# Performance work log

Measured on AMD Instinct MI355X. Metric: run time of the kernel, lower is better.

The kernel has to match this reference:

```python
import jax, jax.numpy as jnp
import numpy as np

B, T, E = 2, 2048, 1024
H = 16
D = E // H  # head_dim = 64


def setup_inputs() -> dict:
    key = jax.random.key(0)
    ks = jax.random.split(key, 9)
    s = 1.0 / np.sqrt(E)
    inp = {"x": jax.random.normal(ks[0], (B, T, E), dtype=jnp.float32)}
    # Linear params (torch nn.Linear: y = x @ W.T + b)
    inp["Wq"] = jax.random.uniform(ks[1], (E, E), jnp.float32, -s, s)
    inp["bq"] = jax.random.uniform(ks[2], (E,), jnp.float32, -s, s)
    inp["Wk"] = jax.random.uniform(ks[3], (E, E), jnp.float32, -s, s)
    inp["bk"] = jax.random.uniform(ks[4], (E,), jnp.float32, -s, s)
    inp["Wv"] = jax.random.uniform(ks[5], (E, E), jnp.float32, -s, s)
    inp["bv"] = jax.random.uniform(ks[6], (E,), jnp.float32, -s, s)
    inp["Wo"] = jax.random.uniform(ks[7], (E, E), jnp.float32, -s, s)
    inp["bo"] = jax.random.uniform(ks[8], (E,), jnp.float32, -s, s)
    return inp


def reference(x, Wq, bq, Wk, bk, Wv, bv, Wo, bo):
    # QKV projections, reshape to [B, H, T, D]
    def split_heads(y):
        return y.reshape(B, T, H, D).transpose(0, 2, 1, 3)

    Q = split_heads(x @ Wq.T + bq)
    K = split_heads(x @ Wk.T + bk)
    V = split_heads(x @ Wv.T + bv)

    scale = 1.0 / jnp.sqrt(jnp.asarray(D, x.dtype))
    scores = jnp.einsum("bhqd,bhkd->bhqk", Q, K) * scale  # [B,H,T,T]
    attn = jax.nn.softmax(scores, axis=-1)
    out = jnp.einsum("bhqk,bhkd->bhqd", attn, V)  # [B,H,T,D]
    out = out.transpose(0, 2, 1, 3).reshape(B, T, E)
    # dropout is identity in eval mode
    return out @ Wo.T + bo
```

## Files before the change

### kernel.cpp

```cpp
#include <hip/hip_runtime.h>
#include <math.h>

#define BB 2
#define TT 2048
#define EE 1024
#define HH 16
#define DD 64
#define MM (BB*TT)
#define KK EE

typedef short bf16x8 __attribute__((ext_vector_type(8)));
typedef float f32x4  __attribute__((ext_vector_type(4)));
typedef float f32x16 __attribute__((ext_vector_type(16)));
typedef unsigned int u32x4 __attribute__((ext_vector_type(4)));

__device__ __forceinline__ unsigned short f2bf(float f) {
  unsigned int u = __float_as_uint(f);
  u = (u + 0x7FFFu + ((u >> 16) & 1u)) >> 16;
  return (unsigned short)u;
}

__device__ __forceinline__ unsigned int cvtpk(float lo, float hi) {
  unsigned int r;
  asm("v_cvt_pk_bf16_f32 %0, %1, %2" : "=v"(r) : "v"(lo), "v"(hi));
  return r;
}

__device__ __forceinline__ void plswap(unsigned int &a, unsigned int &b) {
  asm("v_permlane32_swap_b32 %0, %1" : "+v"(a), "+v"(b));
}

__device__ __forceinline__ void async16(const void* g, void* l) {
  __builtin_amdgcn_global_load_lds(
      (const __attribute__((address_space(1))) unsigned int*)g,
      (__attribute__((address_space(3))) unsigned int*)l, 16, 0, 0);
}

__global__ __launch_bounds__(256) void to_bf16(
    const float* __restrict__ x,  const float* __restrict__ wq,
    const float* __restrict__ wk, const float* __restrict__ wv,
    const float* __restrict__ wo,
    unsigned short* __restrict__ xh, unsigned short* __restrict__ wcat,
    unsigned short* __restrict__ woh)
{
  int c = blockIdx.x * 256 + threadIdx.x;
  const float* src; unsigned short* dst; int off;
  if (c < 1048576) { src = x; dst = xh; off = c; }
  else {
    int r = c - 1048576;
    int w = r >> 18;
    off = r & 262143;
    if      (w == 0) { src = wq; dst = wcat; }
    else if (w == 1) { src = wk; dst = wcat + (1 << 20); }
    else if (w == 2) { src = wv; dst = wcat + (2 << 20); }
    else             { src = wo; dst = woh; }
  }
  float4 v = ((const float4*)src)[off];
  ushort4 h;
  h.x = f2bf(v.x); h.y = f2bf(v.y); h.z = f2bf(v.z); h.w = f2bf(v.w);
  ((ushort4*)dst)[off] = h;
}

template<int MODE>
__global__ __launch_bounds__(512, 6) void gemm_bf16(
    const unsigned short* __restrict__ A, const unsigned short* __restrict__ B,
    const float* __restrict__ b0p, const float* __restrict__ b1p,
    const float* __restrict__ b2p,
    unsigned short* __restrict__ oq, unsigned short* __restrict__ ok,
    unsigned short* __restrict__ ov, float* __restrict__ ofp, float qscale)
{
  constexpr int NT = (MODE == 0) ? 128 : 64;
  constexpr int JN = NT / 32;
  constexpr int BROWS = NT * 32;
  constexpr int TOT = (MODE == 0) ? 16 : 12;
  __shared__ unsigned short S[12288 + 3 * BROWS];

  const int tid  = threadIdx.x;
  const int lane = tid & 63;
  const int wv   = tid >> 6;
  const int col  = lane & 15;
  const int quad = lane >> 4;
  const int wm = (wv & 3) * 32;
  const int wn = (wv >> 2) * (NT / 2);
  const int m0 = blockIdx.x * 128;
  const int n0 = blockIdx.y * NT;

  const int srow = lane >> 2;
  const int sw16 = (((lane & 3) ^ ((lane >> 2) & 3) ^ (lane >> 4)) << 3);
  const int fswA = ((quad ^ (col & 3) ^ (col >> 2)) << 3);

  auto stage = [&](int kt, int slot) {
#pragma unroll
    for (int s = 0; s < 2; ++s) {
      const int t = wv * 2 + s;
      if (t < TOT) {
        const unsigned short* src; int rb, g0, loff;
        if (t < 8) { src = A; rb = t * 16;       g0 = m0; loff = slot * 4096; }
        else       { src = B; rb = (t - 8) * 16; g0 = n0; loff = 12288 + slot * BROWS; }
        async16(src + (size_t)(g0 + rb + srow) * KK + kt + sw16,
                S + loff + rb * 32);
      }
    }
  };

  f32x4 acc[2][JN];
  const f32x4 z = {0.f, 0.f, 0.f, 0.f};
#pragma unroll
  for (int i = 0; i < 2; ++i)
#pragma unroll
    for (int j = 0; j < JN; ++j) acc[i][j] = z;

  stage(0, 0);

#define GBODY(T, SL, S2, DOSTAGE, VMC) do {                                   \
    if (DOSTAGE) stage(((T) + 1) * 32, S2);                                   \
    asm volatile("s_waitcnt vmcnt(" #VMC ")" ::: "memory");                   \
    __builtin_amdgcn_sched_barrier(0);                                        \
    __builtin_amdgcn_s_barrier();                                             \
    __builtin_amdgcn_sched_barrier(0);                                        \
    const unsigned short* Asb = S + (SL) * 4096;                              \
    const unsigned short* Bsb = S + 12288 + (SL) * BROWS;                     \
    bf16x8 bfr[JN];                                                           \
    _Pragma("unroll")                                                         \
    for (int j = 0; j < JN; ++j)                                              \
      bfr[j] = *(const bf16x8*)(Bsb + (wn + j * 16 + col) * 32 + fswA);       \
    _Pragma("unroll")                                                         \
    for (int i = 0; i < 2; ++i) {                                             \
      bf16x8 af = *(const bf16x8*)(Asb + (wm + i * 16 + col) * 32 + fswA);    \
      _Pragma("unroll")                                                       \
      for (int j = 0; j < JN; ++j)                                            \
        acc[i][j] = __builtin_amdgcn_mfma_f32_16x16x32_bf16(af, bfr[j], acc[i][j], 0, 0, 0); \
    }                                                                         \
  } while (0)

  for (int t = 0; t < 30; t += 3) {
    GBODY(t + 0, 0, 1, 1, 2);
    GBODY(t + 1, 1, 2, 1, 2);
    GBODY(t + 2, 2, 0, 1, 2);
  }
  GBODY(30, 0, 1, 1, 2);
  GBODY(31, 1, 0, 0, 0);
#undef GBODY

  unsigned short* Cs = S;
  if (MODE == 0) {
    __syncthreads();
    const int region = n0 >> 10;
    const float* bias = (region == 0) ? b0p : (region == 1) ? b1p : b2p;
    const float scl = (region == 0) ? qscale : 1.0f;
    const int nlbase = n0 & 1023;
    const int h0 = nlbase >> 6;
    const int b = m0 >> 11, t0 = m0 & (TT - 1);
    if (region < 2) {
#pragma unroll
      for (int i = 0; i < 2; ++i)
#pragma unroll
        for (int j = 0; j < 4; ++j) {
          const int nt = wn + j * 16 + col;
          const float bs = bias[nlbase + nt];
#pragma unroll
          for (int r = 0; r < 4; ++r) {
            const int mt = wm + i * 16 + quad * 4 + r;
            Cs[mt * 136 + nt] = f2bf((acc[i][j][r] + bs) * scl);
          }
        }
      __syncthreads();
      unsigned short* dst = (region == 0) ? oq : ok;
#pragma unroll
      for (int s = 0; s < 4; ++s) {
        const int u = s * 512 + tid;
        const int mt = u >> 4, hs = (u >> 3) & 1, ch = u & 7;
        const size_t g = ((size_t)(b * HH + h0 + hs) * TT + t0 + mt) * DD + ch * 8;
        *(uint4*)(dst + g) = *(const uint4*)(Cs + mt * 136 + hs * 64 + ch * 8);
      }
    } else {
#pragma unroll
      for (int i = 0; i < 2; ++i)
#pragma unroll
        for (int j = 0; j < 4; ++j) {
          const int nt = wn + j * 16 + col;
          const float bs = bias[nlbase + nt];
          ushort4 pk;
          pk.x = f2bf(acc[i][j][0] + bs);
          pk.y = f2bf(acc[i][j][1] + bs);
          pk.z = f2bf(acc[i][j][2] + bs);
          pk.w = f2bf(acc[i][j][3] + bs);
          *(ushort4*)(Cs + nt * 136 + wm + i * 16 + quad * 4) = pk;
        }
      __syncthreads();
#pragma unroll
      for (int s = 0; s < 4; ++s) {
        const int u = s * 512 + tid;
        const int nt = u >> 4, ch = u & 15;
        const int d = nt & 63, hs = nt >> 6;
        const size_t g = ((size_t)(b * HH + h0 + hs) * DD + d) * TT + t0 + ch * 8;
        *(uint4*)(ov + g) = *(const uint4*)(Cs + nt * 136 + ch * 8);
      }
    }
  } else {
#pragma unroll
    for (int i = 0; i < 2; ++i) {
#pragma unroll
      for (int j = 0; j < JN; ++j) {
        const int n = n0 + wn + j * 16 + col;
        const float bs = b0p[n];
#pragma unroll
        for (int r = 0; r < 4; ++r) {
          const int m = m0 + wm + i * 16 + quad * 4 + r;
          ofp[(size_t)m * EE + n] = acc[i][j][r] + bs;
        }
      }
    }
  }
}

__global__ __launch_bounds__(512, 6) void gemm_out(
    const unsigned short* __restrict__ A, const unsigned short* __restrict__ B,
    const float* __restrict__ bias, float* __restrict__ ofp)
{
  __shared__ unsigned short S[24576];

  const int tid  = threadIdx.x;
  const int lane = tid & 63;
  const int wv   = tid >> 6;
  const int col  = lane & 15;
  const int quad = lane >> 4;
  const int wm = (wv & 3) * 32;
  const int wn = (wv >> 2) * 32;
  const int m0 = blockIdx.x * 128;
  const int n0 = blockIdx.y * 64;

  const int srow = lane >> 2;
  const int sw16 = (((lane & 3) ^ ((lane >> 2) & 3) ^ (lane >> 4)) << 3);
  const int fswA = ((quad ^ (col & 3) ^ (col >> 2)) << 3);

  auto stage = [&](int kt, int slot) {
#pragma unroll
    for (int s = 0; s < 2; ++s) {
      const int t = wv * 2 + s;
      if (t < 12) {
        const unsigned short* src; int rb, g0, loff;
        if (t < 8) { src = A; rb = t * 16;       g0 = m0; loff = slot * 4096; }
        else       { src = B; rb = (t - 8) * 16; g0 = n0; loff = 16384 + slot * 2048; }
        async16(src + (size_t)(g0 + rb + srow) * KK + kt + sw16,
                S + loff + rb * 32);
      }
    }
  };

  f32x4 acc[2][2];
  const f32x4 z = {0.f, 0.f, 0.f, 0.f};
#pragma unroll
  for (int i = 0; i < 2; ++i)
#pragma unroll
    for (int j = 0; j < 2; ++j) acc[i][j] = z;

  stage(0, 0);
  stage(32, 1);

#define GCOMP(SL) do {                                                        \
    const unsigned short* Asb = S + (SL) * 4096;                              \
    const unsigned short* Bsb = S + 16384 + (SL) * 2048;                      \
    bf16x8 b0 = *(const bf16x8*)(Bsb + (wn + col) * 32 + fswA);               \
    bf16x8 b1 = *(const bf16x8*)(Bsb + (wn + 16 + col) * 32 + fswA);          \
    _Pragma("unroll")                                                         \
    for (int i = 0; i < 2; ++i) {                                             \
      bf16x8 af = *(const bf16x8*)(Asb + (wm + i * 16 + col) * 32 + fswA);    \
      acc[i][0] = __builtin_amdgcn_mfma_f32_16x16x32_bf16(af, b0, acc[i][0], 0, 0, 0); \
      acc[i][1] = __builtin_amdgcn_mfma_f32_16x16x32_bf16(af, b1, acc[i][1], 0, 0, 0); \
    }                                                                         \
} while (0)

#define REGION2(T, SLa, SLb, SSa, SSb, DOSTAGE, VMC) do {                     \
    asm volatile("s_waitcnt vmcnt(" #VMC ")" ::: "memory");                   \
    __builtin_amdgcn_sched_barrier(0);                                        \
    __builtin_amdgcn_s_barrier();                                             \
    __builtin_amdgcn_sched_barrier(0);                                        \
    if (DOSTAGE) { stage(((T) + 2) * 32, SSa); stage(((T) + 3) * 32, SSb); }  \
    GCOMP(SLa);                                                               \
    GCOMP(SLb);                                                               \
} while (0)

  for (int t = 0; t < 28; t += 4) {
    REGION2(t + 0, 0, 1, 2, 3, 1, 0);
    REGION2(t + 2, 2, 3, 0, 1, 1, 0);
  }
  REGION2(28, 0, 1, 2, 3, 1, 0);
  REGION2(30, 2, 3, 0, 1, 0, 0);
#undef REGION2
#undef GCOMP

#pragma unroll
  for (int i = 0; i < 2; ++i) {
#pragma unroll
    for (int j = 0; j < 2; ++j) {
      const int n = n0 + wn + j * 16 + col;
      const float bs = bias[n];
#pragma unroll
      for (int r = 0; r < 4; ++r) {
        const int m = m0 + wm + i * 16 + quad * 4 + r;
        ofp[(size_t)m * EE + n] = acc[i][j][r] + bs;
      }
    }
  }
}

__global__ __launch_bounds__(512, 4) void flash_mfma(
    const unsigned short* __restrict__ Qb, const unsigned short* __restrict__ Kb,
    const unsigned short* __restrict__ Vtb, unsigned short* __restrict__ ctx)
{
  __shared__ unsigned short Qs[128 * 64];
  __shared__ unsigned short Ks[4][64 * 64];
  __shared__ unsigned short Vts[4][64 * 64];

  const int tid  = threadIdx.x;
  const int lane = tid & 63;
  const int wv   = tid >> 6;
  const int lq   = lane & 31;
  const int hf   = lane >> 5;
  const int wq   = wv & 3;
  const int wk2  = wv >> 2;
  const int gid  = blockIdx.x;
  const int bh   = gid & 31;
  const int q0   = (gid >> 5) * 128;

  const unsigned short* Qg = Qb  + (size_t)bh * TT * DD;
  const unsigned short* Kg = Kb  + (size_t)bh * TT * DD;
  const unsigned short* Vg = Vtb + (size_t)bh * DD * TT;

  const int srow = lane >> 3;
  const int swb  = ((lane & 7) ^ (lane >> 3)) << 3;

  const int rbK = wq * 16;
  const bool isK = (wv < 4);
  const int sw0 = swb ^ ((((rbK    ) >> 3) & 7) << 3);
  const int sw1 = swb ^ ((((rbK + 8) >> 3) & 7) << 3);
  const unsigned short* g0 =
      (isK ? Kg + (size_t)(rbK + srow) * DD : Vg + (size_t)(rbK + srow) * TT) + sw0;
  const unsigned short* g1 =
      (isK ? Kg + (size_t)(rbK + 8 + srow) * DD : Vg + (size_t)(rbK + 8 + srow) * TT) + sw1;
  unsigned short* l0 = (isK ? &Ks[0][0] : &Vts[0][0]) + rbK * 64;
  unsigned short* l1 = l0 + 8 * 64;
  const int gstep = isK ? 64 * DD : 64;

  auto stage_kv = [&](int ti, int slot) {
    const size_t go = (size_t)ti * gstep;
    async16(g0 + go, l0 + slot * 4096);
    async16(g1 + go, l1 + slot * 4096);
  };

  const int l7 = lane & 7;
  const int d3 = lq >> 3;
  int koff[4], voff[2][2];
#pragma unroll
  for (int s = 0; s < 4; ++s)
    koff[s] = ((wk2 * 32 + lq) * 64 +
               (((2 * s + hf) ^ l7 ^ ((wk2 * 4 + d3) & 7)) << 3)) * 2;
#pragma unroll
  for (int m = 0; m < 2; ++m)
#pragma unroll
    for (int sg = 0; sg < 2; ++sg)
      voff[m][sg] = ((m * 32 + lq) * 64 +
                     (((wk2 * 4 + 2 * sg + hf) ^ l7 ^ ((m * 4 + d3) & 7)) << 3)) * 2;

#pragma unroll
  for (int s = 0; s < 2; ++s) {
    const int rb = wv * 16 + s * 8;
    const int sq = swb ^ (((rb >> 3) & 7) << 3);
    async16(Qg + (size_t)(q0 + rb + srow) * DD + sq, &Qs[rb * 64]);
  }
  stage_kv(0, 0);
  stage_kv(1, 1);
  __syncthreads();

  bf16x8 aq[4];
#pragma unroll
  for (int s = 0; s < 4; ++s)
    aq[s] = *(const bf16x8*)(Qs + (wq * 32 + lq) * 64 +
                             (((2 * s + hf) ^ l7 ^ ((wq * 4 + d3) & 7)) << 3));

  const f32x16 z16 = {0.f,0.f,0.f,0.f,0.f,0.f,0.f,0.f,
                      0.f,0.f,0.f,0.f,0.f,0.f,0.f,0.f};
  f32x16 o_acc[2];
  o_acc[0] = z16; o_acc[1] = z16;
  float lpart = 0.f;

#define SMPACK(SIN, PA0, PA1) do {                                            \
    {                                                                         \
      float e0 = __builtin_amdgcn_exp2f(SIN[0]);                              \
      float e1 = __builtin_amdgcn_exp2f(SIN[1]);                              \
      float e2 = __builtin_amdgcn_exp2f(SIN[2]);                              \
      float e3 = __builtin_amdgcn_exp2f(SIN[3]);                              \
      float e4 = __builtin_amdgcn_exp2f(SIN[4]);                              \
      float e5 = __builtin_amdgcn_exp2f(SIN[5]);                              \
      float e6 = __builtin_amdgcn_exp2f(SIN[6]);                              \
      float e7 = __builtin_amdgcn_exp2f(SIN[7]);                              \
      lpart += ((e0 + e1) + (e2 + e3)) + ((e4 + e5) + (e6 + e7));             \
      unsigned int a0 = cvtpk(e0, e1), b0 = cvtpk(e4, e5);                    \
      unsigned int a1 = cvtpk(e2, e3), b1 = cvtpk(e6, e7);                    \
      plswap(a0, b0); plswap(a1, b1);                                         \
      u32x4 w = {a0, a1, b0, b1};                                             \
      PA0 = __builtin_bit_cast(bf16x8, w);                                    \
    }                                                                         \
    {                                                                         \
      float e0 = __builtin_amdgcn_exp2f(SIN[8]);                              \
      float e1 = __builtin_amdgcn_exp2f(SIN[9]);                              \
      float e2 = __builtin_amdgcn_exp2f(SIN[10]);                             \
      float e3 = __builtin_amdgcn_exp2f(SIN[11]);                             \
      float e4 = __builtin_amdgcn_exp2f(SIN[12]);                             \
      float e5 = __builtin_amdgcn_exp2f(SIN[13]);                             \
      float e6 = __builtin_amdgcn_exp2f(SIN[14]);                             \
      float e7 = __builtin_amdgcn_exp2f(SIN[15]);                             \
      lpart += ((e0 + e1) + (e2 + e3)) + ((e4 + e5) + (e6 + e7));             \
      unsigned int a0 = cvtpk(e0, e1), b0 = cvtpk(e4, e5);                    \
      unsigned int a1 = cvtpk(e2, e3), b1 = cvtpk(e6, e7);                    \
      plswap(a0, b0); plswap(a1, b1);                                         \
      u32x4 w = {a0, a1, b0, b1};                                             \
      PA1 = __builtin_bit_cast(bf16x8, w);                                    \
    }                                                                         \
} while (0)

#define QKT(SL, SOUT) do {                                                    \
    const char* Kp = (const char*)&Ks[SL][0];                                 \
    bf16x8 ak = *(const bf16x8*)(Kp + koff[0]);                               \
    SOUT = __builtin_amdgcn_mfma_f32_32x32x16_bf16(ak, aq[0], z16, 0, 0, 0);  \
    _Pragma("unroll")                                                         \
    for (int s = 1; s < 4; ++s) {                                             \
      ak = *(const bf16x8*)(Kp + koff[s]);                                    \
      SOUT = __builtin_amdgcn_mfma_f32_32x32x16_bf16(ak, aq[s], SOUT, 0, 0, 0); \
    }                                                                         \
} while (0)

#define PVT(SL, P0, P1) do {                                                  \
    const char* Vp = (const char*)&Vts[SL][0];                                \
    _Pragma("unroll")                                                         \
    for (int m = 0; m < 2; ++m) {                                             \
      bf16x8 v0 = *(const bf16x8*)(Vp + voff[m][0]);                          \
      bf16x8 v1 = *(const bf16x8*)(Vp + voff[m][1]);                          \
      o_acc[m] = __builtin_amdgcn_mfma_f32_32x32x16_bf16(P0, v0, o_acc[m], 0, 0, 0); \
      o_acc[m] = __builtin_amdgcn_mfma_f32_32x32x16_bf16(P1, v1, o_acc[m], 0, 0, 0); \
    }                                                                         \
} while (0)

#define REGION(T, SLa, SLb, SSa, SSb, DOSTAGE) do {                           \
    asm volatile("s_waitcnt vmcnt(0)" ::: "memory");                          \
    __builtin_amdgcn_sched_barrier(0);                                        \
    __builtin_amdgcn_s_barrier();                                             \
    __builtin_amdgcn_sched_barrier(0);                                        \
    if (DOSTAGE) { stage_kv((T) + 2, SSa); stage_kv((T) + 3, SSb); }          \
    f32x16 sa, sb;                                                            \
    __builtin_amdgcn_s_setprio(1);                                            \
    QKT(SLa, sa);                                                             \
    QKT(SLb, sb);                                                             \
    __builtin_amdgcn_s_setprio(0);                                            \
    bf16x8 pa0, pa1, pb0, pb1;                                                \
    SMPACK(sa, pa0, pa1);                                                     \
    __builtin_amdgcn_s_setprio(1);                                            \
    PVT(SLa, pa0, pa1);                                                       \
    __builtin_amdgcn_s_setprio(0);                                            \
    SMPACK(sb, pb0, pb1);                                                     \
    __builtin_amdgcn_s_setprio(1);                                            \
    PVT(SLb, pb0, pb1);                                                       \
    __builtin_amdgcn_s_setprio(0);                                            \
} while (0)

  for (int t = 0; t < 28; t += 4) {
    REGION(t + 0, 0, 1, 2, 3, 1);
    REGION(t + 2, 2, 3, 0, 1, 1);
  }
  REGION(28, 0, 1, 2, 3, 1);
  REGION(30, 2, 3, 0, 1, 0);
#undef REGION
#undef PVT
#undef QKT
#undef SMPACK

  float* Qf = (float*)&Qs[0];
  float* Of = (float*)&Ks[0][0];
  unsigned short* Cs = &Vts[0][0];
  const int bq = bh >> 4, head = bh & 15;

  float lw = lpart + __shfl_xor(lpart, 32);
  if (lane < 32) Qf[wv * 32 + lane] = lw;
  __syncthreads();

  if (wv >= 4) {
#pragma unroll
    for (int m = 0; m < 2; ++m)
#pragma unroll
      for (int r = 0; r < 16; ++r) {
        const int ql = (r & 3) + 8 * (r >> 2) + 4 * hf;
        Of[wq * 2048 + ql * 64 + m * 32 + lq] = o_acc[m][r];
      }
  }
  __syncthreads();

  if (wv < 4) {
    float linv[16];
#pragma unroll
    for (int r = 0; r < 16; ++r) {
      const int ql = (r & 3) + 8 * (r >> 2) + 4 * hf;
      linv[r] = 1.0f / (Qf[wv * 32 + ql] + Qf[(wv + 4) * 32 + ql]);
    }
#pragma unroll
    for (int m = 0; m < 2; ++m)
#pragma unroll
      for (int r = 0; r < 16; ++r) {
        const int ql = (r & 3) + 8 * (r >> 2) + 4 * hf;
        const float val =
            (o_acc[m][r] + Of[wq * 2048 + ql * 64 + m * 32 + lq]) * linv[r];
        const int row = wq * 32 + ql, d = m * 32 + lq;
        Cs[row * 64 + (((d >> 3) ^ (row & 7)) << 3) + (d & 7)] = f2bf(val);
      }
  }
  __syncthreads();

#pragma unroll
  for (int s = 0; s < 2; ++s) {
    const int u = s * 512 + tid;
    const int mr = u >> 3, ch = u & 7;
    const size_t g = ((size_t)(bq * TT + q0 + mr)) * EE + head * DD + ch * 8;
    const int chs = (ch ^ (mr & 7)) << 3;
    *(uint4*)(ctx + g) = *(const uint4*)(Cs + mr * 64 + chs);
  }
}

extern "C" void kernel_launch(void* const* d_in, const int* in_sizes, int n_in,
                              void* d_out, int out_size, void* d_ws, size_t ws_size,
                              hipStream_t stream) {
  const float* x  = (const float*)d_in[0];
  const float* Wq = (const float*)d_in[1];
  const float* bq = (const float*)d_in[2];
  const float* Wk = (const float*)d_in[3];
  const float* bk = (const float*)d_in[4];
  const float* Wv = (const float*)d_in[5];
  const float* bv = (const float*)d_in[6];
  const float* Wo = (const float*)d_in[7];
  const float* bo = (const float*)d_in[8];

  unsigned short* p = (unsigned short*)d_ws;
  const size_t XN = (size_t)MM * EE;
  const size_t WN = (size_t)EE * EE;
  unsigned short* x_h    = p;           p += XN;
  unsigned short* Wcat_h = p;           p += 3 * WN;
  unsigned short* Wo_h   = p;           p += WN;
  unsigned short* Qb     = p;           p += XN;
  unsigned short* Kb     = p;           p += XN;
  unsigned short* Vtb    = p;           p += XN;
  unsigned short* ctx_h  = x_h;

  const float qscale = 0.125f * 1.44269504088896f;

  to_bf16<<<8192, 256, 0, stream>>>(x, Wq, Wk, Wv, Wo, x_h, Wcat_h, Wo_h);

  gemm_bf16<0><<<dim3(MM / 128, 3 * EE / 128), 512, 0, stream>>>(
      x_h, Wcat_h, bq, bk, bv, Qb, Kb, Vtb, nullptr, qscale);

  flash_mfma<<<dim3((TT / 128) * BB * HH), 512, 0, stream>>>(Qb, Kb, Vtb, ctx_h);

  gemm_out<<<dim3(MM / 128, EE / 64), 512, 0, stream>>>(
      ctx_h, Wo_h, bo, (float*)d_out);
}
```

Baseline: 188.7 us.

## Shrink flash attention blocks to 64 queries with double-buffered K/V tiles

The flash attention kernel now runs 256-thread blocks over 64 query rows instead of 512-thread blocks over 128 rows, which doubles the grid. The K/V shared-memory ring drops from four slots to two, and each loop iteration handles a single key tile instead of two interleaved tiles. The goals are lower LDS use per block, more resident blocks and a simpler loop. In exchange, each K/V tile is reloaded from global memory for half as many queries, and the overlap between one tile's softmax and the other tile's MFMA work is lost.

Result: no change. 189.0 us (+0.1%).

```diff
diff --git a/kernel.cpp b/kernel.cpp
--- a/kernel.cpp
+++ b/kernel.cpp
@@ -305,24 +305,24 @@
   }
 }
 
-__global__ __launch_bounds__(512, 4) void flash_mfma(
+__global__ __launch_bounds__(256, 4) void flash_mfma(
     const unsigned short* __restrict__ Qb, const unsigned short* __restrict__ Kb,
     const unsigned short* __restrict__ Vtb, unsigned short* __restrict__ ctx)
 {
-  __shared__ unsigned short Qs[128 * 64];
-  __shared__ unsigned short Ks[4][64 * 64];
-  __shared__ unsigned short Vts[4][64 * 64];
+  __shared__ unsigned short Qs[64 * 64];
+  __shared__ unsigned short Ks[2][64 * 64];
+  __shared__ unsigned short Vts[2][64 * 64];
 
   const int tid  = threadIdx.x;
   const int lane = tid & 63;
   const int wv   = tid >> 6;
   const int lq   = lane & 31;
   const int hf   = lane >> 5;
-  const int wq   = wv & 3;
-  const int wk2  = wv >> 2;
+  const int wq   = wv & 1;
+  const int wk2  = wv >> 1;
   const int gid  = blockIdx.x;
   const int bh   = gid & 31;
-  const int q0   = (gid >> 5) * 128;
+  const int q0   = (gid >> 5) * 64;
 
   const unsigned short* Qg = Qb  + (size_t)bh * TT * DD;
   const unsigned short* Kg = Kb  + (size_t)bh * TT * DD;
@@ -331,22 +331,25 @@
   const int srow = lane >> 3;
   const int swb  = ((lane & 7) ^ (lane >> 3)) << 3;
 
-  const int rbK = wq * 16;
-  const bool isK = (wv < 4);
-  const int sw0 = swb ^ ((((rbK    ) >> 3) & 7) << 3);
-  const int sw1 = swb ^ ((((rbK + 8) >> 3) & 7) << 3);
-  const unsigned short* g0 =
-      (isK ? Kg + (size_t)(rbK + srow) * DD : Vg + (size_t)(rbK + srow) * TT) + sw0;
-  const unsigned short* g1 =
-      (isK ? Kg + (size_t)(rbK + 8 + srow) * DD : Vg + (size_t)(rbK + 8 + srow) * TT) + sw1;
-  unsigned short* l0 = (isK ? &Ks[0][0] : &Vts[0][0]) + rbK * 64;
-  unsigned short* l1 = l0 + 8 * 64;
+  const bool isK = (wv < 2);
+  const int rbase = (wv & 1) * 32;
+  const unsigned short* gp[4];
+  unsigned short* lp[4];
+#pragma unroll
+  for (int s = 0; s < 4; ++s) {
+    const int rb = rbase + s * 8;
+    const int sw = swb ^ (((rb >> 3) & 7) << 3);
+    gp[s] = (isK ? Kg + (size_t)(rb + srow) * DD
+                 : Vg + (size_t)(rb + srow) * TT) + sw;
+    lp[s] = (isK ? &Ks[0][0] : &Vts[0][0]) + rb * 64;
+  }
   const int gstep = isK ? 64 * DD : 64;
 
   auto stage_kv = [&](int ti, int slot) {
     const size_t go = (size_t)ti * gstep;
-    async16(g0 + go, l0 + slot * 4096);
-    async16(g1 + go, l1 + slot * 4096);
+#pragma unroll
+    for (int s = 0; s < 4; ++s)
+      async16(gp[s] + go, lp[s] + slot * 4096);
   };
 
   const int l7 = lane & 7;
@@ -370,7 +373,6 @@
     async16(Qg + (size_t)(q0 + rb + srow) * DD + sq, &Qs[rb * 64]);
   }
   stage_kv(0, 0);
-  stage_kv(1, 1);
   __syncthreads();
 
   bf16x8 aq[4];
@@ -385,95 +387,77 @@
   o_acc[0] = z16; o_acc[1] = z16;
   float lpart = 0.f;
 
-#define SMPACK(SIN, PA0, PA1) do {                                            \
-    {                                                                         \
-      float e0 = __builtin_amdgcn_exp2f(SIN[0]);                              \
-      float e1 = __builtin_amdgcn_exp2f(SIN[1]);                              \
-      float e2 = __builtin_amdgcn_exp2f(SIN[2]);                              \
-      float e3 = __builtin_amdgcn_exp2f(SIN[3]);                              \
-      float e4 = __builtin_amdgcn_exp2f(SIN[4]);                              \
-      float e5 = __builtin_amdgcn_exp2f(SIN[5]);                              \
-      float e6 = __builtin_amdgcn_exp2f(SIN[6]);                              \
-      float e7 = __builtin_amdgcn_exp2f(SIN[7]);                              \
+#define BODY(T, SL) do {                                                      \
+    asm volatile("s_waitcnt vmcnt(0)" ::: "memory");                          \
+    __builtin_amdgcn_sched_barrier(0);                                        \
+    __builtin_amdgcn_s_barrier();                                             \
+    __builtin_amdgcn_sched_barrier(0);                                        \
+    if ((T) + 1 < 32) stage_kv((T) + 1, (SL) ^ 1);                            \
+    f32x16 sacc;                                                              \
+    {                \
+      const char* Kp = (const char*)&Ks[SL][0];                               \
+      bf16x8 ak = *(const bf16x8*)(Kp + koff[0]);                             \
+      __builtin_amdgcn_s_setprio(1);                                          \
+      sacc = __builtin_amdgcn_mfma_f32_32x32x16_bf16(ak, aq[0], z16, 0, 0, 0);\
+      _Pragma("unroll")                                                       \
+      for (int s = 1; s < 4; ++s) {                                           \
+        ak = *(const bf16x8*)(Kp + koff[s]);                                  \
+        sacc = __builtin_amdgcn_mfma_f32_32x32x16_bf16(ak, aq[s], sacc, 0, 0, 0); \
+      }                                                                       \
+      __builtin_amdgcn_s_setprio(0);                                          \
+    }                                                                         \
+    bf16x8 pa0, pa1;                                                          \
+    {                     \
+      float e0 = __builtin_amdgcn_exp2f(sacc[0]);                             \
+      float e1 = __builtin_amdgcn_exp2f(sacc[1]);                             \
+      float e2 = __builtin_amdgcn_exp2f(sacc[2]);                             \
+      float e3 = __builtin_amdgcn_exp2f(sacc[3]);                             \
+      float e4 = __builtin_amdgcn_exp2f(sacc[4]);                             \
+      float e5 = __builtin_amdgcn_exp2f(sacc[5]);                             \
+      float e6 = __builtin_amdgcn_exp2f(sacc[6]);                             \
+      float e7 = __builtin_amdgcn_exp2f(sacc[7]);                             \
       lpart += ((e0 + e1) + (e2 + e3)) + ((e4 + e5) + (e6 + e7));             \
       unsigned int a0 = cvtpk(e0, e1), b0 = cvtpk(e4, e5);                    \
       unsigned int a1 = cvtpk(e2, e3), b1 = cvtpk(e6, e7);                    \
       plswap(a0, b0); plswap(a1, b1);                                         \
       u32x4 w = {a0, a1, b0, b1};                                             \
-      PA0 = __builtin_bit_cast(bf16x8, w);                                    \
+      pa0 = __builtin_bit_cast(bf16x8, w);                                    \
     }                                                                         \
-    {                                                                         \
-      float e0 = __builtin_amdgcn_exp2f(SIN[8]);                              \
-      float e1 = __builtin_amdgcn_exp2f(SIN[9]);                              \
-      float e2 = __builtin_amdgcn_exp2f(SIN[10]);                             \
-      float e3 = __builtin_amdgcn_exp2f(SIN[11]);                             \
-      float e4 = __builtin_amdgcn_exp2f(SIN[12]);                             \
-      float e5 = __builtin_amdgcn_exp2f(SIN[13]);                             \
-      float e6 = __builtin_amdgcn_exp2f(SIN[14]);                             \
-      float e7 = __builtin_amdgcn_exp2f(SIN[15]);                             \
+    {                                                     \
+      float e0 = __builtin_amdgcn_exp2f(sacc[8]);                             \
+      float e1 = __builtin_amdgcn_exp2f(sacc[9]);                             \
+      float e2 = __builtin_amdgcn_exp2f(sacc[10]);                            \
+      float e3 = __builtin_amdgcn_exp2f(sacc[11]);                            \
+      float e4 = __builtin_amdgcn_exp2f(sacc[12]);                            \
+      float e5 = __builtin_amdgcn_exp2f(sacc[13]);                            \
+      float e6 = __builtin_amdgcn_exp2f(sacc[14]);                            \
+      float e7 = __builtin_amdgcn_exp2f(sacc[15]);                            \
       lpart += ((e0 + e1) + (e2 + e3)) + ((e4 + e5) + (e6 + e7));             \
       unsigned int a0 = cvtpk(e0, e1), b0 = cvtpk(e4, e5);                    \
       unsigned int a1 = cvtpk(e2, e3), b1 = cvtpk(e6, e7);                    \
       plswap(a0, b0); plswap(a1, b1);                                         \
       u32x4 w = {a0, a1, b0, b1};                                             \
-      PA1 = __builtin_bit_cast(bf16x8, w);                                    \
+      pa1 = __builtin_bit_cast(bf16x8, w);                                    \
+    }                                                                         \
+    {                                                              \
+      const char* Vp = (const char*)&Vts[SL][0];                              \
+      __builtin_amdgcn_s_setprio(1);                                          \
+      _Pragma("unroll")                                                       \
+      for (int m = 0; m < 2; ++m) {                                           \
+        bf16x8 v0 = *(const bf16x8*)(Vp + voff[m][0]);                        \
+        bf16x8 v1 = *(const bf16x8*)(Vp + voff[m][1]);                        \
+        o_acc[m] = __builtin_amdgcn_mfma_f32_32x32x16_bf16(pa0, v0, o_acc[m], 0, 0, 0); \
+        o_acc[m] = __builtin_amdgcn_mfma_f32_32x32x16_bf16(pa1, v1, o_acc[m], 0, 0, 0); \
+      }                                                                       \
+      __builtin_amdgcn_s_setprio(0);                                          \
     }                                                                         \
 } while (0)
 
-#define QKT(SL, SOUT) do {                                                    \
-    const char* Kp = (const char*)&Ks[SL][0];                                 \
-    bf16x8 ak = *(const bf16x8*)(Kp + koff[0]);                               \
-    SOUT = __builtin_amdgcn_mfma_f32_32x32x16_bf16(ak, aq[0], z16, 0, 0, 0);  \
-    _Pragma("unroll")                                                         \
-    for (int s = 1; s < 4; ++s) {                                             \
-      ak = *(const bf16x8*)(Kp + koff[s]);                                    \
-      SOUT = __builtin_amdgcn_mfma_f32_32x32x16_bf16(ak, aq[s], SOUT, 0, 0, 0); \
-    }                                                                         \
-} while (0)
-
-#define PVT(SL, P0, P1) do {                                                  \
-    const char* Vp = (const char*)&Vts[SL][0];                                \
-    _Pragma("unroll")                                                         \
-    for (int m = 0; m < 2; ++m) {                                             \
-      bf16x8 v0 = *(const bf16x8*)(Vp + voff[m][0]);                          \
-      bf16x8 v1 = *(const bf16x8*)(Vp + voff[m][1]);                          \
-      o_acc[m] = __builtin_amdgcn_mfma_f32_32x32x16_bf16(P0, v0, o_acc[m], 0, 0, 0); \
-      o_acc[m] = __builtin_amdgcn_mfma_f32_32x32x16_bf16(P1, v1, o_acc[m], 0, 0, 0); \
-    }                                                                         \
-} while (0)
-
-#define REGION(T, SLa, SLb, SSa, SSb, DOSTAGE) do {                           \
-    asm volatile("s_waitcnt vmcnt(0)" ::: "memory");                          \
-    __builtin_amdgcn_sched_barrier(0);                                        \
-    __builtin_amdgcn_s_barrier();                                             \
-    __builtin_amdgcn_sched_barrier(0);                                        \
-    if (DOSTAGE) { stage_kv((T) + 2, SSa); stage_kv((T) + 3, SSb); }          \
-    f32x16 sa, sb;                                                            \
-    __builtin_amdgcn_s_setprio(1);                                            \
-    QKT(SLa, sa);                                                             \
-    QKT(SLb, sb);                                                             \
-    __builtin_amdgcn_s_setprio(0);                                            \
-    bf16x8 pa0, pa1, pb0, pb1;                                                \
-    SMPACK(sa, pa0, pa1);                                                     \
-    __builtin_amdgcn_s_setprio(1);                                            \
-    PVT(SLa, pa0, pa1);                                                       \
-    __builtin_amdgcn_s_setprio(0);                                            \
-    SMPACK(sb, pb0, pb1);                                                     \
-    __builtin_amdgcn_s_setprio(1);                                            \
-    PVT(SLb, pb0, pb1);                                                       \
-    __builtin_amdgcn_s_setprio(0);                                            \
-} while (0)
-
-  for (int t = 0; t < 28; t += 4) {
-    REGION(t + 0, 0, 1, 2, 3, 1);
-    REGION(t + 2, 2, 3, 0, 1, 1);
-  }
-  REGION(28, 0, 1, 2, 3, 1);
-  REGION(30, 2, 3, 0, 1, 0);
-#undef REGION
-#undef PVT
-#undef QKT
-#undef SMPACK
+  for (int t = 0; t < 32; t += 2) {
+    BODY(t, 0);
+    BODY(t + 1, 1);
+  }
+#undef BODY
 
   float* Qf = (float*)&Qs[0];
   float* Of = (float*)&Ks[0][0];
@@ -484,7 +468,7 @@
   if (lane < 32) Qf[wv * 32 + lane] = lw;
   __syncthreads();
 
-  if (wv >= 4) {
+  if (wv >= 2) {
 #pragma unroll
     for (int m = 0; m < 2; ++m)
 #pragma unroll
@@ -495,12 +479,12 @@
   }
   __syncthreads();
 
-  if (wv < 4) {
+  if (wv < 2) {
     float linv[16];
 #pragma unroll
     for (int r = 0; r < 16; ++r) {
       const int ql = (r & 3) + 8 * (r >> 2) + 4 * hf;
-      linv[r] = 1.0f / (Qf[wv * 32 + ql] + Qf[(wv + 4) * 32 + ql]);
+      linv[r] = 1.0f / (Qf[wv * 32 + ql] + Qf[(wv + 2) * 32 + ql]);
     }
 #pragma unroll
     for (int m = 0; m < 2; ++m)
@@ -517,7 +501,7 @@
 
 #pragma unroll
   for (int s = 0; s < 2; ++s) {
-    const int u = s * 512 + tid;
+    const int u = s * 256 + tid;
     const int mr = u >> 3, ch = u & 7;
     const size_t g = ((size_t)(bq * TT + q0 + mr)) * EE + head * DD + ch * 8;
     const int chs = (ch ^ (mr & 7)) << 3;
@@ -556,7 +540,7 @@
   gemm_bf16<0><<<dim3(MM / 128, 3 * EE / 128), 512, 0, stream>>>(
       x_h, Wcat_h, bq, bk, bv, Qb, Kb, Vtb, nullptr, qscale);
 
-  flash_mfma<<<dim3((TT / 128) * BB * HH), 512, 0, stream>>>(Qb, Kb, Vtb, ctx_h);
+  flash_mfma<<<dim3((TT / 64) * BB * HH), 256, 0, stream>>>(Qb, Kb, Vtb, ctx_h);
 
   gemm_out<<<dim3(MM / 128, EE / 64), 512, 0, stream>>>(
       ctx_h, Wo_h, bo, (float*)d_out);
```
